# Kernel tuning notes

Hardware: AMD Instinct MI355X
Metric: run time of the kernel (lower is better)

Reference implementation:

```python
import jax, jax.numpy as jnp
import numpy as np

H = 1024        # hidden_size
E = 3           # num_smear experts
DI = 1280       # int(1.25 * H), GRU inner dim (expansion_factor=1.25)
EPS = 1e-6


def setup_inputs() -> dict:
    key = jax.random.key(0)
    ks = jax.random.split(key, 5)
    B, S = 4, 4096
    s = 0.02
    return {
        "inputs": jax.random.normal(ks[0], (B, S, H), jnp.float32),
        "norm_weight": jnp.ones((H,), jnp.float32),
        "router_w": jax.random.normal(ks[1], (H, E), jnp.float32) * s,
        "router_b": jnp.zeros((E,), jnp.float32),
        "w_in": jax.random.normal(ks[2], (E, H, 2 * DI), jnp.float32) * s,
        "b_in": jnp.zeros((E, 2 * DI), jnp.float32),
        "w_out": jax.random.normal(ks[3], (E, DI, H), jnp.float32) * s,
        "b_out": jnp.zeros((E, H), jnp.float32),
    }


def _g(x):
    # minGRU candidate activation: x + 0.5 for x >= 0, sigmoid(x) otherwise
    return jnp.where(x >= 0, x + 0.5, jax.nn.sigmoid(x))


def reference(inputs, norm_weight, router_w, router_b, w_in, b_in, w_out, b_out):
    B, S, _ = inputs.shape
    # RMSNorm
    x = inputs * jax.lax.rsqrt(jnp.mean(inputs * inputs, axis=-1, keepdims=True) + EPS)
    x = x * norm_weight

    # SMEAR routing: softmax over experts from mean-pooled tokens, per sample
    pooled = x.mean(axis=1)                                   # [B, H]
    probs = jax.nn.softmax(pooled @ router_w + router_b, -1)  # [B, E]

    # Soft-merge expert parameters per sample
    Wi = jnp.einsum('be,edh->bdh', probs, w_in)    # [B, H, 2*DI]
    bi = jnp.einsum('be,eh->bh', probs, b_in)      # [B, 2*DI]
    Wo = jnp.einsum('be,edh->bdh', probs, w_out)   # [B, DI, H]
    bo = jnp.einsum('be,eh->bh', probs, b_out)     # [B, H]

    # GRU (minGRU) input projection
    zh = jnp.einsum('bsd,bdh->bsh', x, Wi) + bi[:, None, :]   # [B, S, 2*DI]
    hid, gate = jnp.split(zh, 2, axis=-1)
    z = jax.nn.sigmoid(gate)   # update gate [B, S, DI]
    ht = _g(hid)               # candidate    [B, S, DI]

    def step(h, zt_ht):
        z_t, ht_t = zt_ht
        h = (1.0 - z_t) * h + z_t * ht_t
        return h, h

    h0 = jnp.zeros((B, DI), x.dtype)
    _, hs = jax.lax.scan(step, h0, (z.swapaxes(0, 1), ht.swapaxes(0, 1)))
    hs = hs.swapaxes(0, 1)     # [B, S, DI]

    out = jnp.einsum('bsh,bhd->bsd', hs, Wo) + bo[:, None, :]  # proj_out
    out = out + inputs                                          # residual (dropout=0, eval)
    new_state = hs[:, -1]                                       # [B, DI]
    aux_loss = jnp.zeros((), inputs.dtype)
    return out, new_state, aux_loss
```

## Files before the change

### kernel.cpp

```cpp
#include <hip/hip_runtime.h>
#include <hip/hip_bf16.h>

#define B_  4
#define S_  4096
#define H_  1024
#define DI_ 1280
#define DI2_ 2560
#define E_  3
#define NC_ 64
#define CL_ 64
#define EPS_ 1e-6f

typedef unsigned short ushort_t;
typedef __attribute__((ext_vector_type(8))) __bf16 bf16x8;
typedef __attribute__((ext_vector_type(4))) float f32x4;

__device__ inline ushort_t f2bf(float f) {
    union { float f; unsigned u; } v; v.f = f;
    unsigned r = v.u + 0x7fffu + ((v.u >> 16) & 1u);
    return (ushort_t)(r >> 16);
}
__device__ inline float bf2f(ushort_t s) {
    union { unsigned u; float f; } v; v.u = ((unsigned)s) << 16;
    return v.f;
}
__device__ inline float sigmoidf_(float x) { return 1.0f / (1.0f + __expf(-x)); }

__device__ inline void gld16(const void* g, void* l) {
    __builtin_amdgcn_global_load_lds(
        (const __attribute__((address_space(1))) void*)g,
        (__attribute__((address_space(3))) void*)l, 16, 0, 0);
}

__global__ __launch_bounds__(256) void rmsnorm_kernel(
    const float* __restrict__ in, const float* __restrict__ nw,
    ushort_t* __restrict__ xbf, float* __restrict__ partial)
{
    int g = blockIdx.x, b = blockIdx.y;
    int tid = threadIdx.x, lane = tid & 63, w = tid >> 6;
    int s0 = g * 16;
    const float4* inb = (const float4*)(in + ((size_t)b * S_ + s0) * H_);
    float4 rows[16];
    float ss[16];
#pragma unroll
    for (int r = 0; r < 16; r++) {
        float4 v = inb[(size_t)r * (H_ / 4) + tid];
        rows[r] = v;
        ss[r] = v.x * v.x + v.y * v.y + v.z * v.z + v.w * v.w;
    }
#pragma unroll
    for (int r = 0; r < 16; r++) {
        float s = ss[r];
        s += __shfl_down(s, 32); s += __shfl_down(s, 16); s += __shfl_down(s, 8);
        s += __shfl_down(s, 4);  s += __shfl_down(s, 2);  s += __shfl_down(s, 1);
        ss[r] = s;
    }
    __shared__ float red[16][4];
    __shared__ float scl[16];
    if (lane == 0) {
#pragma unroll
        for (int r = 0; r < 16; r++) red[r][w] = ss[r];
    }
    __syncthreads();
    if (tid < 16) {
        float t = red[tid][0] + red[tid][1] + red[tid][2] + red[tid][3];
        scl[tid] = rsqrtf(t * (1.0f / H_) + EPS_);
    }
    __syncthreads();
    float4 nw4 = ((const float4*)nw)[tid];
    float4 pacc = {0.f, 0.f, 0.f, 0.f};
    ushort_t* xrow = xbf + ((size_t)b * S_ + s0) * H_;
#pragma unroll
    for (int r = 0; r < 16; r++) {
        float sc = scl[r];
        float4 v = rows[r];
        v.x = v.x * sc * nw4.x; v.y = v.y * sc * nw4.y;
        v.z = v.z * sc * nw4.z; v.w = v.w * sc * nw4.w;
        ushort4 u; u.x = f2bf(v.x); u.y = f2bf(v.y); u.z = f2bf(v.z); u.w = f2bf(v.w);
        *(ushort4*)(xrow + (size_t)r * H_ + tid * 4) = u;
        pacc.x += v.x; pacc.y += v.y; pacc.z += v.z; pacc.w += v.w;
    }
    float4* pp = (float4*)(partial + ((size_t)(b * 256 + g)) * H_);
    pp[tid] = pacc;
}

__global__ __launch_bounds__(256) void router_kernel(
    const float* __restrict__ partial, const float* __restrict__ rw,
    const float* __restrict__ rb, const float* __restrict__ b_in,
    const float* __restrict__ b_out, float* __restrict__ probs,
    float* __restrict__ bi, float* __restrict__ bo, float* __restrict__ aux)
{
    int b = blockIdx.x;
    int tid = threadIdx.x, lane = tid & 63, w = tid >> 6;
    float4 acc = {0.f, 0.f, 0.f, 0.f};
    const float4* pp = (const float4*)partial;
    for (int g = 0; g < 256; g++) {
        float4 v = pp[((size_t)(b * 256 + g)) * (H_ / 4) + tid];
        acc.x += v.x; acc.y += v.y; acc.z += v.z; acc.w += v.w;
    }
    const float inv_s = 1.0f / (float)S_;
    float a4[4] = {acc.x * inv_s, acc.y * inv_s, acc.z * inv_s, acc.w * inv_s};
    float le[3] = {0.f, 0.f, 0.f};
    int h0 = tid * 4;
#pragma unroll
    for (int j = 0; j < 4; j++) {
        float p = a4[j];
        le[0] += p * rw[(size_t)(h0 + j) * 3 + 0];
        le[1] += p * rw[(size_t)(h0 + j) * 3 + 1];
        le[2] += p * rw[(size_t)(h0 + j) * 3 + 2];
    }
#pragma unroll
    for (int e = 0; e < 3; e++) {
        float s = le[e];
        s += __shfl_down(s, 32); s += __shfl_down(s, 16); s += __shfl_down(s, 8);
        s += __shfl_down(s, 4);  s += __shfl_down(s, 2);  s += __shfl_down(s, 1);
        le[e] = s;
    }
    __shared__ float red[4][3];
    __shared__ float pr[3];
    if (lane == 0) { red[w][0] = le[0]; red[w][1] = le[1]; red[w][2] = le[2]; }
    __syncthreads();
    if (tid == 0) {
        float l0 = red[0][0] + red[1][0] + red[2][0] + red[3][0] + rb[0];
        float l1 = red[0][1] + red[1][1] + red[2][1] + red[3][1] + rb[1];
        float l2 = red[0][2] + red[1][2] + red[2][2] + red[3][2] + rb[2];
        float m = fmaxf(l0, fmaxf(l1, l2));
        float e0 = __expf(l0 - m), e1 = __expf(l1 - m), e2 = __expf(l2 - m);
        float inv = 1.0f / (e0 + e1 + e2);
        pr[0] = e0 * inv; pr[1] = e1 * inv; pr[2] = e2 * inv;
    }
    __syncthreads();
    if (tid < 3) probs[b * 3 + tid] = pr[tid];
    float p0 = pr[0], p1 = pr[1], p2 = pr[2];
    for (int n = tid; n < DI2_; n += 256)
        bi[(size_t)b * DI2_ + n] = p0 * b_in[n] + p1 * b_in[DI2_ + n] + p2 * b_in[2 * DI2_ + n];
    for (int n = tid; n < H_; n += 256)
        bo[(size_t)b * H_ + n] = p0 * b_out[n] + p1 * b_out[H_ + n] + p2 * b_out[2 * H_ + n];
    if (b == 0 && tid == 0) *aux = 0.0f;
}

__global__ __launch_bounds__(256) void mix_kernel(
    const float* __restrict__ wsrc, const float* __restrict__ probs,
    ushort_t* __restrict__ dst, int K, int N)
{
    int kt = blockIdx.x, nt = blockIdx.y, b = blockIdx.z;
    float p0 = probs[b * 3 + 0], p1 = probs[b * 3 + 1], p2 = probs[b * 3 + 2];
    __shared__ float T[64][65];
    int tid = threadIdx.x;
    int c = tid & 63, rr = tid >> 6;
    const float* w0 = wsrc;
    const float* w1 = wsrc + (size_t)K * N;
    const float* w2 = wsrc + 2 * (size_t)K * N;
    int k0 = kt * 64, n0 = nt * 64;
#pragma unroll
    for (int pass = 0; pass < 16; pass++) {
        int r = pass * 4 + rr;
        size_t idx = (size_t)(k0 + r) * N + n0 + c;
        T[r][c] = p0 * w0[idx] + p1 * w1[idx] + p2 * w2[idx];
    }
    __syncthreads();
    ushort_t* db = dst + (size_t)b * N * K;
#pragma unroll
    for (int pass = 0; pass < 16; pass++) {
        int j = pass * 4 + rr;
        db[(size_t)(n0 + j) * K + k0 + c] = f2bf(T[c][j]);
    }
}

template <int MODE>
__global__ __launch_bounds__(256, 2) void gemm_bt(
    const ushort_t* __restrict__ Aall, const ushort_t* __restrict__ Btall,
    int M, int N, int K,
    const float* __restrict__ biasAll,
    const float* __restrict__ resAll, float* __restrict__ outAll,
    ushort_t* __restrict__ htAll, ushort_t* __restrict__ zAll, int DIv)
{
    __shared__ ushort_t As[128 * 32];
    __shared__ ushort_t Bs[128 * 32];
    int b = blockIdx.z;
    const ushort_t* A = Aall + (size_t)b * M * K;
    const ushort_t* Bt = Btall + (size_t)b * N * K;
    int tid = threadIdx.x, lane = tid & 63, w = tid >> 6;
    int mblk = blockIdx.x * 128, nblk = blockIdx.y * 128;

    int srow = lane >> 2;
    int sblk = (lane & 3) ^ ((srow >> 1) & 3);
    int scol = sblk * 8;
    const ushort_t* ga0 = A + (size_t)(mblk + (w * 2 + 0) * 16 + srow) * K + scol;
    const ushort_t* ga1 = A + (size_t)(mblk + (w * 2 + 1) * 16 + srow) * K + scol;
    const ushort_t* gb0 = Bt + (size_t)(nblk + (w * 2 + 0) * 16 + srow) * K + scol;
    const ushort_t* gb1 = Bt + (size_t)(nblk + (w * 2 + 1) * 16 + srow) * K + scol;
    ushort_t* la0 = &As[(w * 2 + 0) * 512 + lane * 8];
    ushort_t* la1 = &As[(w * 2 + 1) * 512 + lane * 8];
    ushort_t* lb0 = &Bs[(w * 2 + 0) * 512 + lane * 8];
    ushort_t* lb1 = &Bs[(w * 2 + 1) * 512 + lane * 8];

    f32x4 acc[4][4] = {};
    int wy = w & 1, wx = w >> 1;
    int q = lane >> 4;
    int ml = lane & 15;
    int rblk = (q ^ ((ml >> 1) & 3)) * 8;
    int aoff0 = wy * 2048 + ml * 32 + rblk;
    int boff0 = wx * 2048 + ml * 32 + rblk;

    for (int k0 = 0; k0 < K; k0 += 32) {
        gld16(ga0, la0); gld16(ga1, la1);
        gld16(gb0, lb0); gld16(gb1, lb1);
        ga0 += 32; ga1 += 32; gb0 += 32; gb1 += 32;
        __syncthreads();
        bf16x8 af[4], bfr[4];
#pragma unroll
        for (int i = 0; i < 4; i++) af[i] = *(const bf16x8*)&As[aoff0 + i * 512];
#pragma unroll
        for (int i = 0; i < 4; i++) bfr[i] = *(const bf16x8*)&Bs[boff0 + i * 512];
#pragma unroll
        for (int mi = 0; mi < 4; mi++)
#pragma unroll
            for (int ni = 0; ni < 4; ni++)
                acc[mi][ni] = __builtin_amdgcn_mfma_f32_16x16x32_bf16(bfr[ni], af[mi], acc[mi][ni], 0, 0, 0);
        __syncthreads();
    }

    int nq = nblk + wx * 64 + q * 4;
    const float* bias = biasAll + (size_t)b * N;
    if (MODE == 0) {
        bool isgate = (nblk >= DIv);
        ushort_t* dst = (isgate ? zAll : htAll) + (size_t)b * (size_t)M * DIv;
        int ncol0 = isgate ? (nq - DIv) : nq;
#pragma unroll
        for (int mi = 0; mi < 4; mi++) {
            int m = mblk + wy * 64 + mi * 16 + ml;
            ushort_t* drow = dst + (size_t)m * DIv;
#pragma unroll
            for (int ni = 0; ni < 4; ni++) {
                float4 bv = *(const float4*)&bias[nq + ni * 16];
                f32x4 a = acc[mi][ni];
                float v0 = a[0] + bv.x, v1 = a[1] + bv.y, v2 = a[2] + bv.z, v3 = a[3] + bv.w;
                float r0, r1, r2, r3;
                if (isgate) {
                    r0 = sigmoidf_(v0); r1 = sigmoidf_(v1); r2 = sigmoidf_(v2); r3 = sigmoidf_(v3);
                } else {
                    r0 = (v0 >= 0.f) ? (v0 + 0.5f) : sigmoidf_(v0);
                    r1 = (v1 >= 0.f) ? (v1 + 0.5f) : sigmoidf_(v1);
                    r2 = (v2 >= 0.f) ? (v2 + 0.5f) : sigmoidf_(v2);
                    r3 = (v3 >= 0.f) ? (v3 + 0.5f) : sigmoidf_(v3);
                }
                ushort4 u; u.x = f2bf(r0); u.y = f2bf(r1); u.z = f2bf(r2); u.w = f2bf(r3);
                *(ushort4*)&drow[ncol0 + ni * 16] = u;
            }
        }
    } else {
        const float* resb = resAll + (size_t)b * (size_t)M * N;
        float* outp = outAll + (size_t)b * (size_t)M * N;
#pragma unroll
        for (int mi = 0; mi < 4; mi++) {
            int m = mblk + wy * 64 + mi * 16 + ml;
            const float* rrow = resb + (size_t)m * N;
            float* orow = outp + (size_t)m * N;
#pragma unroll
            for (int ni = 0; ni < 4; ni++) {
                int n0 = nq + ni * 16;
                float4 bv = *(const float4*)&bias[n0];
                float4 rv = *(const float4*)&rrow[n0];
                f32x4 a = acc[mi][ni];
                float4 o;
                o.x = a[0] + bv.x + rv.x; o.y = a[1] + bv.y + rv.y;
                o.z = a[2] + bv.z + rv.z; o.w = a[3] + bv.w + rv.w;
                *(float4*)&orow[n0] = o;
            }
        }
    }
}

__global__ __launch_bounds__(320) void scan_phase1(
    const ushort_t* __restrict__ zb, const ushort_t* __restrict__ hb,
    float* __restrict__ cA, float* __restrict__ cB)
{
    int d0 = threadIdx.x * 4;
    int c = blockIdx.x, b = blockIdx.y;
    size_t base = ((size_t)b * S_ + (size_t)c * CL_) * DI_ + d0;
    float A[4] = {1.f, 1.f, 1.f, 1.f};
    float Bc[4] = {0.f, 0.f, 0.f, 0.f};
    for (int t = 0; t < CL_; t++) {
        ushort4 zv = *(const ushort4*)&zb[base + (size_t)t * DI_];
        ushort4 hv = *(const ushort4*)&hb[base + (size_t)t * DI_];
        float z[4] = {bf2f(zv.x), bf2f(zv.y), bf2f(zv.z), bf2f(zv.w)};
        float h[4] = {bf2f(hv.x), bf2f(hv.y), bf2f(hv.z), bf2f(hv.w)};
#pragma unroll
        for (int j = 0; j < 4; j++) {
            float a = 1.f - z[j];
            A[j] *= a;
            Bc[j] = a * Bc[j] + z[j] * h[j];
        }
    }
    size_t o = ((size_t)b * NC_ + c) * DI_ + d0;
    float4 av; av.x = A[0]; av.y = A[1]; av.z = A[2]; av.w = A[3];
    float4 bv; bv.x = Bc[0]; bv.y = Bc[1]; bv.z = Bc[2]; bv.w = Bc[3];
    *(float4*)&cA[o] = av;
    *(float4*)&cB[o] = bv;
}

__global__ __launch_bounds__(256) void scan_phase2(
    const float* __restrict__ cA, const float* __restrict__ cB,
    float* __restrict__ h0buf, float* __restrict__ ns)
{
    int g = blockIdx.x * 256 + threadIdx.x;
    int b = g / (DI_ / 4), dq = g % (DI_ / 4);
    int d0 = dq * 4;
    float4 h = {0.f, 0.f, 0.f, 0.f};
    for (int c = 0; c < NC_; c++) {
        size_t o = ((size_t)b * NC_ + c) * DI_ + d0;
        *(float4*)&h0buf[o] = h;
        float4 a = *(const float4*)&cA[o];
        float4 bb = *(const float4*)&cB[o];
        h.x = a.x * h.x + bb.x; h.y = a.y * h.y + bb.y;
        h.z = a.z * h.z + bb.z; h.w = a.w * h.w + bb.w;
    }
    *(float4*)&ns[(size_t)b * DI_ + d0] = h;
}

__global__ __launch_bounds__(320) void scan_phase3(
    const ushort_t* __restrict__ zb, const ushort_t* __restrict__ hb,
    const float* __restrict__ h0buf, ushort_t* __restrict__ hs)
{
    int d0 = threadIdx.x * 4;
    int c = blockIdx.x, b = blockIdx.y;
    size_t base = ((size_t)b * S_ + (size_t)c * CL_) * DI_ + d0;
    float4 h0 = *(const float4*)&h0buf[((size_t)b * NC_ + c) * DI_ + d0];
    float h[4] = {h0.x, h0.y, h0.z, h0.w};
    for (int t = 0; t < CL_; t++) {
        ushort4 zv = *(const ushort4*)&zb[base + (size_t)t * DI_];
        ushort4 hv = *(const ushort4*)&hb[base + (size_t)t * DI_];
        float z[4] = {bf2f(zv.x), bf2f(zv.y), bf2f(zv.z), bf2f(zv.w)};
        float ht[4] = {bf2f(hv.x), bf2f(hv.y), bf2f(hv.z), bf2f(hv.w)};
        ushort4 u;
        h[0] = (1.f - z[0]) * h[0] + z[0] * ht[0]; u.x = f2bf(h[0]);
        h[1] = (1.f - z[1]) * h[1] + z[1] * ht[1]; u.y = f2bf(h[1]);
        h[2] = (1.f - z[2]) * h[2] + z[2] * ht[2]; u.z = f2bf(h[2]);
        h[3] = (1.f - z[3]) * h[3] + z[3] * ht[3]; u.w = f2bf(h[3]);
        *(ushort4*)&hs[base + (size_t)t * DI_] = u;
    }
}

extern "C" void kernel_launch(void* const* d_in, const int* in_sizes, int n_in,
                              void* d_out, int out_size, void* d_ws, size_t ws_size,
                              hipStream_t stream)
{
    const float* in    = (const float*)d_in[0];
    const float* nw    = (const float*)d_in[1];
    const float* rw    = (const float*)d_in[2];
    const float* rb    = (const float*)d_in[3];
    const float* w_in  = (const float*)d_in[4];
    const float* b_in  = (const float*)d_in[5];
    const float* w_out = (const float*)d_in[6];
    const float* b_out = (const float*)d_in[7];
    float* out = (float*)d_out;

    char* ws = (char*)d_ws;
    size_t off = 0;
    auto nxt = [&](size_t bytes) -> void* {
        void* p = ws + off;
        off += (bytes + 255) & ~(size_t)255;
        return p;
    };
    ushort_t* xbf    = (ushort_t*)nxt((size_t)B_ * S_ * H_ * 2);
    ushort_t* wi_t   = (ushort_t*)nxt((size_t)B_ * DI2_ * H_ * 2);
    ushort_t* wo_t   = (ushort_t*)nxt((size_t)B_ * H_ * DI_ * 2);
    ushort_t* zbuf   = (ushort_t*)nxt((size_t)B_ * S_ * DI_ * 2);
    ushort_t* htbuf  = (ushort_t*)nxt((size_t)B_ * S_ * DI_ * 2);
    ushort_t* hsbuf  = (ushort_t*)nxt((size_t)B_ * S_ * DI_ * 2);
    float* partial   = (float*)nxt((size_t)B_ * 256 * H_ * 4);
    float* probs     = (float*)nxt((size_t)B_ * 3 * 4);
    float* bi        = (float*)nxt((size_t)B_ * DI2_ * 4);
    float* bo        = (float*)nxt((size_t)B_ * H_ * 4);
    float* cA        = (float*)nxt((size_t)B_ * NC_ * DI_ * 4);
    float* cB        = (float*)nxt((size_t)B_ * NC_ * DI_ * 4);
    float* h0buf     = (float*)nxt((size_t)B_ * NC_ * DI_ * 4);

    float* ns  = out + (size_t)B_ * S_ * H_;
    float* aux = ns + (size_t)B_ * DI_;

    rmsnorm_kernel<<<dim3(S_ / 16, B_), 256, 0, stream>>>(in, nw, xbf, partial);
    router_kernel<<<dim3(B_), 256, 0, stream>>>(partial, rw, rb, b_in, b_out, probs, bi, bo, aux);
    mix_kernel<<<dim3(H_ / 64, DI2_ / 64, B_), 256, 0, stream>>>(w_in, probs, wi_t, H_, DI2_);
    mix_kernel<<<dim3(DI_ / 64, H_ / 64, B_), 256, 0, stream>>>(w_out, probs, wo_t, DI_, H_);
    gemm_bt<0><<<dim3(S_ / 128, DI2_ / 128, B_), 256, 0, stream>>>(
        xbf, wi_t, S_, DI2_, H_, bi, nullptr, nullptr, htbuf, zbuf, DI_);
    scan_phase1<<<dim3(NC_, B_), 320, 0, stream>>>(zbuf, htbuf, cA, cB);
    scan_phase2<<<dim3(5), 256, 0, stream>>>(cA, cB, h0buf, ns);
    scan_phase3<<<dim3(NC_, B_), 320, 0, stream>>>(zbuf, htbuf, h0buf, hsbuf);
    gemm_bt<1><<<dim3(S_ / 128, H_ / 128, B_), 256, 0, stream>>>(
        hsbuf, wo_t, S_, H_, DI_, bo, in, out, nullptr, nullptr, DI_);
    (void)in_sizes; (void)n_in; (void)out_size; (void)ws_size;
}
```

Before: 436.2 us.

## Interleave hid/gate columns, deepen GEMM K-step, swizzle tiles, parallelize router reduction

Result: no change. 428.1 us (-1.8%).

```diff
diff --git a/kernel.cpp b/kernel.cpp
--- a/kernel.cpp
+++ b/kernel.cpp
@@ -84,8 +84,21 @@
     pp[tid] = pacc;
 }
 
+__global__ __launch_bounds__(256) void reduce_kernel(
+    const float* __restrict__ partial, float* __restrict__ partial2)
+{
+    int b = blockIdx.x, j = blockIdx.y, tid = threadIdx.x;
+    float4 acc = {0.f, 0.f, 0.f, 0.f};
+    const float4* pp = (const float4*)partial;
+    for (int g = j * 32; g < j * 32 + 32; g++) {
+        float4 v = pp[((size_t)(b * 256 + g)) * (H_ / 4) + tid];
+        acc.x += v.x; acc.y += v.y; acc.z += v.z; acc.w += v.w;
+    }
+    ((float4*)partial2)[((size_t)(b * 8 + j)) * (H_ / 4) + tid] = acc;
+}
+
 __global__ __launch_bounds__(256) void router_kernel(
-    const float* __restrict__ partial, const float* __restrict__ rw,
+    const float* __restrict__ partial2, const float* __restrict__ rw,
     const float* __restrict__ rb, const float* __restrict__ b_in,
     const float* __restrict__ b_out, float* __restrict__ probs,
     float* __restrict__ bi, float* __restrict__ bo, float* __restrict__ aux)
@@ -93,9 +106,9 @@
     int b = blockIdx.x;
     int tid = threadIdx.x, lane = tid & 63, w = tid >> 6;
     float4 acc = {0.f, 0.f, 0.f, 0.f};
-    const float4* pp = (const float4*)partial;
-    for (int g = 0; g < 256; g++) {
-        float4 v = pp[((size_t)(b * 256 + g)) * (H_ / 4) + tid];
+    const float4* pp = (const float4*)partial2;
+    for (int g = 0; g < 8; g++) {
+        float4 v = pp[((size_t)(b * 8 + g)) * (H_ / 4) + tid];
         acc.x += v.x; acc.y += v.y; acc.z += v.z; acc.w += v.w;
     }
     const float inv_s = 1.0f / (float)S_;
@@ -132,8 +145,11 @@
     __syncthreads();
     if (tid < 3) probs[b * 3 + tid] = pr[tid];
     float p0 = pr[0], p1 = pr[1], p2 = pr[2];
-    for (int n = tid; n < DI2_; n += 256)
-        bi[(size_t)b * DI2_ + n] = p0 * b_in[n] + p1 * b_in[DI2_ + n] + p2 * b_in[2 * DI2_ + n];
+    for (int n = tid; n < DI2_; n += 256) {
+        int d = n >> 1;
+        int src = (n & 1) ? (DI_ + d) : d;
+        bi[(size_t)b * DI2_ + n] = p0 * b_in[src] + p1 * b_in[DI2_ + src] + p2 * b_in[2 * DI2_ + src];
+    }
     for (int n = tid; n < H_; n += 256)
         bo[(size_t)b * H_ + n] = p0 * b_out[n] + p1 * b_out[H_ + n] + p2 * b_out[2 * H_ + n];
     if (b == 0 && tid == 0) *aux = 0.0f;
@@ -167,21 +183,65 @@
     }
 }
 
+__global__ __launch_bounds__(256) void mix_in_kernel(
+    const float* __restrict__ wsrc, const float* __restrict__ probs,
+    ushort_t* __restrict__ dst)
+{
+    int kt = blockIdx.x, dt = blockIdx.y, b = blockIdx.z;
+    float p0 = probs[b * 3 + 0], p1 = probs[b * 3 + 1], p2 = probs[b * 3 + 2];
+    __shared__ float Th[64][33];
+    __shared__ float Tg[64][33];
+    int tid = threadIdx.x;
+    int k0 = kt * 64, d0 = dt * 32;
+    const float* w0 = wsrc;
+    const float* w1 = wsrc + (size_t)H_ * DI2_;
+    const float* w2 = wsrc + 2 * (size_t)H_ * DI2_;
+    {
+        int c = tid & 31, rr = tid >> 5;
+#pragma unroll
+        for (int pass = 0; pass < 8; pass++) {
+            int r = pass * 8 + rr;
+            size_t ih = (size_t)(k0 + r) * DI2_ + d0 + c;
+            size_t ig = ih + DI_;
+            Th[r][c] = p0 * w0[ih] + p1 * w1[ih] + p2 * w2[ih];
+            Tg[r][c] = p0 * w0[ig] + p1 * w1[ig] + p2 * w2[ig];
+        }
+    }
+    __syncthreads();
+    ushort_t* db = dst + (size_t)b * DI2_ * H_;
+    int n0i = d0 * 2;
+    int c = tid & 63, rr = tid >> 6;
+#pragma unroll
+    for (int pass = 0; pass < 16; pass++) {
+        int jj = pass * 4 + rr;
+        int d = jj >> 1;
+        float v = (jj & 1) ? Tg[c][d] : Th[c][d];
+        db[(size_t)(n0i + jj) * H_ + k0 + c] = f2bf(v);
+    }
+}
+
 template <int MODE>
 __global__ __launch_bounds__(256, 2) void gemm_bt(
     const ushort_t* __restrict__ Aall, const ushort_t* __restrict__ Btall,
     int M, int N, int K,
     const float* __restrict__ biasAll,
     const float* __restrict__ resAll, float* __restrict__ outAll,
-    ushort_t* __restrict__ htAll, ushort_t* __restrict__ zAll, int DIv)
-{
-    __shared__ ushort_t As[128 * 32];
-    __shared__ ushort_t Bs[128 * 32];
+    ushort_t* __restrict__ zhAll)
+{
+    __shared__ ushort_t As[2 * 128 * 32];
+    __shared__ ushort_t Bs[2 * 128 * 32];
     int b = blockIdx.z;
     const ushort_t* A = Aall + (size_t)b * M * K;
     const ushort_t* Bt = Btall + (size_t)b * N * K;
     int tid = threadIdx.x, lane = tid & 63, w = tid >> 6;
-    int mblk = blockIdx.x * 128, nblk = blockIdx.y * 128;
+
+    int num_n = N >> 7;
+    const int GROUP = 4;
+    int gsz = GROUP * num_n;
+    int gid = blockIdx.x / gsz, rem = blockIdx.x % gsz;
+    int mt = gid * GROUP + (rem & (GROUP - 1));
+    int nt = rem >> 2;
+    int mblk = mt * 128, nblk = nt * 128;
 
     int srow = lane >> 2;
     int sblk = (lane & 3) ^ ((srow >> 1) & 3);
@@ -203,50 +263,49 @@
     int aoff0 = wy * 2048 + ml * 32 + rblk;
     int boff0 = wx * 2048 + ml * 32 + rblk;
 
-    for (int k0 = 0; k0 < K; k0 += 32) {
-        gld16(ga0, la0); gld16(ga1, la1);
-        gld16(gb0, lb0); gld16(gb1, lb1);
-        ga0 += 32; ga1 += 32; gb0 += 32; gb1 += 32;
+    for (int k0 = 0; k0 < K; k0 += 64) {
+        gld16(ga0, la0);       gld16(ga1, la1);
+        gld16(gb0, lb0);       gld16(gb1, lb1);
+        gld16(ga0 + 32, la0 + 4096); gld16(ga1 + 32, la1 + 4096);
+        gld16(gb0 + 32, lb0 + 4096); gld16(gb1 + 32, lb1 + 4096);
+        ga0 += 64; ga1 += 64; gb0 += 64; gb1 += 64;
         __syncthreads();
-        bf16x8 af[4], bfr[4];
-#pragma unroll
-        for (int i = 0; i < 4; i++) af[i] = *(const bf16x8*)&As[aoff0 + i * 512];
-#pragma unroll
-        for (int i = 0; i < 4; i++) bfr[i] = *(const bf16x8*)&Bs[boff0 + i * 512];
-#pragma unroll
-        for (int mi = 0; mi < 4; mi++)
-#pragma unroll
-            for (int ni = 0; ni < 4; ni++)
-                acc[mi][ni] = __builtin_amdgcn_mfma_f32_16x16x32_bf16(bfr[ni], af[mi], acc[mi][ni], 0, 0, 0);
+#pragma unroll
+        for (int p = 0; p < 2; p++) {
+            bf16x8 af[4], bfr[4];
+#pragma unroll
+            for (int i = 0; i < 4; i++) af[i] = *(const bf16x8*)&As[p * 4096 + aoff0 + i * 512];
+#pragma unroll
+            for (int i = 0; i < 4; i++) bfr[i] = *(const bf16x8*)&Bs[p * 4096 + boff0 + i * 512];
+#pragma unroll
+            for (int mi = 0; mi < 4; mi++)
+#pragma unroll
+                for (int ni = 0; ni < 4; ni++)
+                    acc[mi][ni] = __builtin_amdgcn_mfma_f32_16x16x32_bf16(bfr[ni], af[mi], acc[mi][ni], 0, 0, 0);
+        }
         __syncthreads();
     }
 
     int nq = nblk + wx * 64 + q * 4;
     const float* bias = biasAll + (size_t)b * N;
     if (MODE == 0) {
-        bool isgate = (nblk >= DIv);
-        ushort_t* dst = (isgate ? zAll : htAll) + (size_t)b * (size_t)M * DIv;
-        int ncol0 = isgate ? (nq - DIv) : nq;
+        ushort_t* dst = zhAll + (size_t)b * (size_t)M * N;
 #pragma unroll
         for (int mi = 0; mi < 4; mi++) {
             int m = mblk + wy * 64 + mi * 16 + ml;
-            ushort_t* drow = dst + (size_t)m * DIv;
+            ushort_t* drow = dst + (size_t)m * N;
 #pragma unroll
             for (int ni = 0; ni < 4; ni++) {
-                float4 bv = *(const float4*)&bias[nq + ni * 16];
+                int n0 = nq + ni * 16;
+                float4 bv = *(const float4*)&bias[n0];
                 f32x4 a = acc[mi][ni];
-                float v0 = a[0] + bv.x, v1 = a[1] + bv.y, v2 = a[2] + bv.z, v3 = a[3] + bv.w;
-                float r0, r1, r2, r3;
-                if (isgate) {
-                    r0 = sigmoidf_(v0); r1 = sigmoidf_(v1); r2 = sigmoidf_(v2); r3 = sigmoidf_(v3);
-                } else {
-                    r0 = (v0 >= 0.f) ? (v0 + 0.5f) : sigmoidf_(v0);
-                    r1 = (v1 >= 0.f) ? (v1 + 0.5f) : sigmoidf_(v1);
-                    r2 = (v2 >= 0.f) ? (v2 + 0.5f) : sigmoidf_(v2);
-                    r3 = (v3 >= 0.f) ? (v3 + 0.5f) : sigmoidf_(v3);
-                }
-                ushort4 u; u.x = f2bf(r0); u.y = f2bf(r1); u.z = f2bf(r2); u.w = f2bf(r3);
-                *(ushort4*)&drow[ncol0 + ni * 16] = u;
+                float h0 = a[0] + bv.x, z0 = a[1] + bv.y;
+                float h1 = a[2] + bv.z, z1 = a[3] + bv.w;
+                float ht0 = (h0 >= 0.f) ? (h0 + 0.5f) : sigmoidf_(h0);
+                float ht1 = (h1 >= 0.f) ? (h1 + 0.5f) : sigmoidf_(h1);
+                float zz0 = sigmoidf_(z0), zz1 = sigmoidf_(z1);
+                ushort4 u; u.x = f2bf(ht0); u.y = f2bf(zz0); u.z = f2bf(ht1); u.w = f2bf(zz1);
+                *(ushort4*)&drow[n0] = u;
             }
         }
     } else {
@@ -273,24 +332,23 @@
 }
 
 __global__ __launch_bounds__(320) void scan_phase1(
-    const ushort_t* __restrict__ zb, const ushort_t* __restrict__ hb,
-    float* __restrict__ cA, float* __restrict__ cB)
+    const ushort_t* __restrict__ zh, float* __restrict__ cA, float* __restrict__ cB)
 {
     int d0 = threadIdx.x * 4;
     int c = blockIdx.x, b = blockIdx.y;
-    size_t base = ((size_t)b * S_ + (size_t)c * CL_) * DI_ + d0;
+    const ushort_t* base = zh + ((size_t)b * S_ + (size_t)c * CL_) * DI2_ + d0 * 2;
     float A[4] = {1.f, 1.f, 1.f, 1.f};
     float Bc[4] = {0.f, 0.f, 0.f, 0.f};
     for (int t = 0; t < CL_; t++) {
-        ushort4 zv = *(const ushort4*)&zb[base + (size_t)t * DI_];
-        ushort4 hv = *(const ushort4*)&hb[base + (size_t)t * DI_];
-        float z[4] = {bf2f(zv.x), bf2f(zv.y), bf2f(zv.z), bf2f(zv.w)};
-        float h[4] = {bf2f(hv.x), bf2f(hv.y), bf2f(hv.z), bf2f(hv.w)};
+        uint4 u = *(const uint4*)(base + (size_t)t * DI2_);
+        unsigned uu[4] = {u.x, u.y, u.z, u.w};
 #pragma unroll
         for (int j = 0; j < 4; j++) {
-            float a = 1.f - z[j];
+            float ht = bf2f((ushort_t)(uu[j] & 0xffff));
+            float z  = bf2f((ushort_t)(uu[j] >> 16));
+            float a = 1.f - z;
             A[j] *= a;
-            Bc[j] = a * Bc[j] + z[j] * h[j];
+            Bc[j] = a * Bc[j] + z * ht;
         }
     }
     size_t o = ((size_t)b * NC_ + c) * DI_ + d0;
@@ -320,25 +378,27 @@
 }
 
 __global__ __launch_bounds__(320) void scan_phase3(
-    const ushort_t* __restrict__ zb, const ushort_t* __restrict__ hb,
-    const float* __restrict__ h0buf, ushort_t* __restrict__ hs)
+    const ushort_t* __restrict__ zh, const float* __restrict__ h0buf,
+    ushort_t* __restrict__ hs)
 {
     int d0 = threadIdx.x * 4;
     int c = blockIdx.x, b = blockIdx.y;
-    size_t base = ((size_t)b * S_ + (size_t)c * CL_) * DI_ + d0;
+    const ushort_t* base = zh + ((size_t)b * S_ + (size_t)c * CL_) * DI2_ + d0 * 2;
+    ushort_t* hbase = hs + ((size_t)b * S_ + (size_t)c * CL_) * DI_ + d0;
     float4 h0 = *(const float4*)&h0buf[((size_t)b * NC_ + c) * DI_ + d0];
     float h[4] = {h0.x, h0.y, h0.z, h0.w};
     for (int t = 0; t < CL_; t++) {
-        ushort4 zv = *(const ushort4*)&zb[base + (size_t)t * DI_];
-        ushort4 hv = *(const ushort4*)&hb[base + (size_t)t * DI_];
-        float z[4] = {bf2f(zv.x), bf2f(zv.y), bf2f(zv.z), bf2f(zv.w)};
-        float ht[4] = {bf2f(hv.x), bf2f(hv.y), bf2f(hv.z), bf2f(hv.w)};
-        ushort4 u;
-        h[0] = (1.f - z[0]) * h[0] + z[0] * ht[0]; u.x = f2bf(h[0]);
-        h[1] = (1.f - z[1]) * h[1] + z[1] * ht[1]; u.y = f2bf(h[1]);
-        h[2] = (1.f - z[2]) * h[2] + z[2] * ht[2]; u.z = f2bf(h[2]);
-        h[3] = (1.f - z[3]) * h[3] + z[3] * ht[3]; u.w = f2bf(h[3]);
-        *(ushort4*)&hs[base + (size_t)t * DI_] = u;
+        uint4 u = *(const uint4*)(base + (size_t)t * DI2_);
+        unsigned uu[4] = {u.x, u.y, u.z, u.w};
+        ushort4 o;
+#pragma unroll
+        for (int j = 0; j < 4; j++) {
+            float ht = bf2f((ushort_t)(uu[j] & 0xffff));
+            float z  = bf2f((ushort_t)(uu[j] >> 16));
+            h[j] = (1.f - z) * h[j] + z * ht;
+        }
+        o.x = f2bf(h[0]); o.y = f2bf(h[1]); o.z = f2bf(h[2]); o.w = f2bf(h[3]);
+        *(ushort4*)(hbase + (size_t)t * DI_) = o;
     }
 }
 
@@ -366,10 +426,10 @@
     ushort_t* xbf    = (ushort_t*)nxt((size_t)B_ * S_ * H_ * 2);
     ushort_t* wi_t   = (ushort_t*)nxt((size_t)B_ * DI2_ * H_ * 2);
     ushort_t* wo_t   = (ushort_t*)nxt((size_t)B_ * H_ * DI_ * 2);
-    ushort_t* zbuf   = (ushort_t*)nxt((size_t)B_ * S_ * DI_ * 2);
-    ushort_t* htbuf  = (ushort_t*)nxt((size_t)B_ * S_ * DI_ * 2);
+    ushort_t* zhbuf  = (ushort_t*)nxt((size_t)B_ * S_ * DI2_ * 2);
     ushort_t* hsbuf  = (ushort_t*)nxt((size_t)B_ * S_ * DI_ * 2);
     float* partial   = (float*)nxt((size_t)B_ * 256 * H_ * 4);
+    float* partial2  = (float*)nxt((size_t)B_ * 8 * H_ * 4);
     float* probs     = (float*)nxt((size_t)B_ * 3 * 4);
     float* bi        = (float*)nxt((size_t)B_ * DI2_ * 4);
     float* bo        = (float*)nxt((size_t)B_ * H_ * 4);
@@ -381,15 +441,16 @@
     float* aux = ns + (size_t)B_ * DI_;
 
     rmsnorm_kernel<<<dim3(S_ / 16, B_), 256, 0, stream>>>(in, nw, xbf, partial);
-    router_kernel<<<dim3(B_), 256, 0, stream>>>(partial, rw, rb, b_in, b_out, probs, bi, bo, aux);
-    mix_kernel<<<dim3(H_ / 64, DI2_ / 64, B_), 256, 0, stream>>>(w_in, probs, wi_t, H_, DI2_);
+    reduce_kernel<<<dim3(B_, 8), 256, 0, stream>>>(partial, partial2);
+    router_kernel<<<dim3(B_), 256, 0, stream>>>(partial2, rw, rb, b_in, b_out, probs, bi, bo, aux);
+    mix_in_kernel<<<dim3(H_ / 64, DI_ / 32, B_), 256, 0, stream>>>(w_in, probs, wi_t);
     mix_kernel<<<dim3(DI_ / 64, H_ / 64, B_), 256, 0, stream>>>(w_out, probs, wo_t, DI_, H_);
-    gemm_bt<0><<<dim3(S_ / 128, DI2_ / 128, B_), 256, 0, stream>>>(
-        xbf, wi_t, S_, DI2_, H_, bi, nullptr, nullptr, htbuf, zbuf, DI_);
-    scan_phase1<<<dim3(NC_, B_), 320, 0, stream>>>(zbuf, htbuf, cA, cB);
+    gemm_bt<0><<<dim3((S_ / 128) * (DI2_ / 128), 1, B_), 256, 0, stream>>>(
+        xbf, wi_t, S_, DI2_, H_, bi, nullptr, nullptr, zhbuf);
+    scan_phase1<<<dim3(NC_, B_), 320, 0, stream>>>(zhbuf, cA, cB);
     scan_phase2<<<dim3(5), 256, 0, stream>>>(cA, cB, h0buf, ns);
-    scan_phase3<<<dim3(NC_, B_), 320, 0, stream>>>(zbuf, htbuf, h0buf, hsbuf);
-    gemm_bt<1><<<dim3(S_ / 128, H_ / 128, B_), 256, 0, stream>>>(
-        hsbuf, wo_t, S_, H_, DI_, bo, in, out, nullptr, nullptr, DI_);
+    scan_phase3<<<dim3(NC_, B_), 320, 0, stream>>>(zhbuf, h0buf, hsbuf);
+    gemm_bt<1><<<dim3((S_ / 128) * (H_ / 128), 1, B_), 256, 0, stream>>>(
+        hsbuf, wo_t, S_, H_, DI_, bo, in, out, nullptr);
     (void)in_sizes; (void)n_in; (void)out_size; (void)ws_size;
 }
```
